# Kernel optimization log

Measured on AMD Instinct MI355X. Metric: run time of the kernel, lower is better.

## Reference

```python
import jax, jax.numpy as jnp
import numpy as np

HEADS, MAX_SEQ, N_STATE = 8, 2048, 512
DEPTH = N_STATE // HEADS
B, S = 2, 2048
EPS = 1e-5


def setup_inputs() -> dict:
    key = jax.random.key(0)
    ks = jax.random.split(key, 8)
    sd = lambda f: 1.0 / np.sqrt(f)
    causal = jnp.tril(jnp.ones((S, S), dtype=bool))
    mask = jnp.where(causal, 0.0, -1e9).astype(jnp.float32)[None, None]
    return {
        "x": jax.random.normal(ks[0], (B, S, N_STATE), jnp.float32),
        "mask": mask,
        "W_qkv": jax.random.normal(ks[1], (N_STATE, 3 * N_STATE), jnp.float32) * sd(N_STATE),
        "b_qkv": jnp.zeros((3 * N_STATE,), jnp.float32),
        "W_proj": jax.random.normal(ks[2], (N_STATE, N_STATE), jnp.float32) * sd(N_STATE),
        "b_proj": jnp.zeros((N_STATE,), jnp.float32),
        "E": jax.random.normal(ks[3], (HEADS, MAX_SEQ, DEPTH), jnp.float32) * sd(DEPTH),
        "g1": jnp.ones((N_STATE,), jnp.float32),
        "be1": jnp.zeros((N_STATE,), jnp.float32),
        "g2": jnp.ones((N_STATE,), jnp.float32),
        "be2": jnp.zeros((N_STATE,), jnp.float32),
        "W_fc1": jax.random.normal(ks[4], (N_STATE, 4 * N_STATE), jnp.float32) * sd(N_STATE),
        "b_fc1": jnp.zeros((4 * N_STATE,), jnp.float32),
        "W_fc2": jax.random.normal(ks[5], (4 * N_STATE, N_STATE), jnp.float32) * sd(4 * N_STATE),
        "b_fc2": jnp.zeros((N_STATE,), jnp.float32),
    }


def _layernorm(x, g, b):
    mu = jnp.mean(x, axis=-1, keepdims=True)
    var = jnp.mean(jnp.square(x - mu), axis=-1, keepdims=True)
    return (x - mu) * jax.lax.rsqrt(var + EPS) * g + b


def _relative_skew(rel):
    # rel: [B, H, S, S] = q @ E_slice^T ; skew trick -> relative positions
    b, h, s, _ = rel.shape
    rel = jnp.pad(rel, ((0, 0), (0, 0), (0, 0), (1, 0)))  # [B,H,S,S+1]
    rel = rel.reshape(b, h, s + 1, s)
    return rel[:, :, 1:, :]  # [B,H,S,S]


def reference(x, mask, W_qkv, b_qkv, W_proj, b_proj, E, g1, be1, g2, be2,
              W_fc1, b_fc1, W_fc2, b_fc2):
    b, s, _ = x.shape
    a = _layernorm(x, g1, be1)
    qkv = a @ W_qkv + b_qkv  # [B,S,3N]
    q, k, v = jnp.split(qkv, 3, axis=-1)
    split = lambda t: t.reshape(b, s, HEADS, DEPTH).transpose(0, 2, 1, 3)  # [B,H,S,D]
    q, k, v = split(q), split(k), split(v)
    present = jnp.stack([k, v], axis=1)  # [B,2,H,S,D]

    w = jnp.einsum("bhqd,bhkd->bhqk", q, k)
    E_s = E[:, MAX_SEq if False else MAX_SEQ - s:, :]  # [H,S,D]
    rel = jnp.einsum("bhqd,hld->bhql", q, E_s)
    w = (w + _relative_skew(rel)) * (1.0 / np.sqrt(DEPTH))
    w = w + mask
    w = jax.nn.softmax(w, axis=-1)
    att = jnp.einsum("bhqk,bhkd->bhqd", w, v)
    att = att.transpose(0, 2, 1, 3).reshape(b, s, N_STATE)
    att = att @ W_proj + b_proj

    x = x + att
    m = _layernorm(x, g2, be2)
    m = jax.nn.gelu(m @ W_fc1 + b_fc1) @ W_fc2 + b_fc2
    x = x + m
    return (x, present)
```

## Files before the change

kernel.cpp:

```cpp
#include <hip/hip_runtime.h>
#include <stdint.h>

#define DEV __device__ __forceinline__

typedef __attribute__((ext_vector_type(8))) short bf16x8;
typedef __attribute__((ext_vector_type(4))) float f32x4;

DEV ushort f2bf(float f) {
  union { float f; uint32_t u; } c; c.f = f;
  return (ushort)((c.u + 0x7FFFu + ((c.u >> 16) & 1)) >> 16);
}
DEV bf16x8 ld8(const ushort* p) { return *reinterpret_cast<const bf16x8*>(p); }

DEV void gload16(const void* g, void* l) {
  __builtin_amdgcn_global_load_lds(
      (const __attribute__((address_space(1))) uint32_t*)g,
      (__attribute__((address_space(3))) uint32_t*)l, 16, 0, 0);
}

__global__ __launch_bounds__(256) void k_transpose_bf(const float* __restrict__ in,
                                                      ushort* __restrict__ out,
                                                      int R, int C) {
  __shared__ float t[32][33];
  int tx = threadIdx.x & 31, ty = threadIdx.x >> 5;
  int c0 = blockIdx.x * 32, r0 = blockIdx.y * 32;
#pragma unroll
  for (int k = 0; k < 4; ++k)
    t[ty + 8 * k][tx] = in[(size_t)(r0 + ty + 8 * k) * C + c0 + tx];
  __syncthreads();
#pragma unroll
  for (int k = 0; k < 4; ++k)
    out[(size_t)(c0 + ty + 8 * k) * R + r0 + tx] = f2bf(t[tx][ty + 8 * k]);
}

__global__ __launch_bounds__(256) void k_cvt_bf(const float* __restrict__ in,
                                                ushort* __restrict__ out, int n4) {
  int i = blockIdx.x * 256 + threadIdx.x;
  if (i >= n4) return;
  float4 v = reinterpret_cast<const float4*>(in)[i];
  ushort4 o; o.x = f2bf(v.x); o.y = f2bf(v.y); o.z = f2bf(v.z); o.w = f2bf(v.w);
  reinterpret_cast<ushort4*>(out)[i] = o;
}

__global__ __launch_bounds__(256) void k_ln(const float* __restrict__ x,
                                            const float* __restrict__ g,
                                            const float* __restrict__ be,
                                            ushort* __restrict__ out) {
  int w = threadIdx.x >> 6, lane = threadIdx.x & 63;
  int row = blockIdx.x * 4 + w;
  const float* xr = x + (size_t)row * 512 + lane * 8;
  float4 a = *reinterpret_cast<const float4*>(xr);
  float4 b = *reinterpret_cast<const float4*>(xr + 4);
  float xs[8] = {a.x, a.y, a.z, a.w, b.x, b.y, b.z, b.w};
  float s = 0.f, q = 0.f;
#pragma unroll
  for (int i = 0; i < 8; ++i) { s += xs[i]; q += xs[i] * xs[i]; }
#pragma unroll
  for (int off = 32; off; off >>= 1) { s += __shfl_xor(s, off); q += __shfl_xor(q, off); }
  float mu = s * (1.f / 512.f);
  float var = q * (1.f / 512.f) - mu * mu;
  float inv = rsqrtf(var + 1e-5f);
  const float* gp = g + lane * 8;
  const float* bp = be + lane * 8;
  ushort o[8];
#pragma unroll
  for (int i = 0; i < 8; ++i) o[i] = f2bf((xs[i] - mu) * inv * gp[i] + bp[i]);
  *reinterpret_cast<uint4*>(out + (size_t)row * 512 + lane * 8) = *reinterpret_cast<uint4*>(o);
}

template <int EPI, int BN>
__global__ __launch_bounds__(256) void k_gemm(
    const ushort* __restrict__ A, const ushort* __restrict__ Bt,
    int M, int N, int K,
    const float* __restrict__ bias, const float* __restrict__ res,
    float* __restrict__ outf, ushort* __restrict__ outb,
    float* __restrict__ present, ushort* __restrict__ qbf,
    ushort* __restrict__ kbf, ushort* __restrict__ vtbf) {
  constexpr int NF = BN / 32;
  __shared__ ushort As[2][128][64];
  __shared__ ushort Bs[2][BN][64];
  const int tid = threadIdx.x, lane = tid & 63, w = tid >> 6;
  const int g = lane >> 4, l16 = lane & 15;
  const int m0 = blockIdx.y * 128, n0 = blockIdx.x * BN;
  const int wm = (w >> 1) * 64, wn = (w & 1) * (BN / 2);
  f32x4 acc[4][NF];
#pragma unroll
  for (int i = 0; i < 4; ++i)
#pragma unroll
    for (int j = 0; j < NF; ++j) acc[i][j] = (f32x4){0.f, 0.f, 0.f, 0.f};

  const int lrow_off = (lane << 4);
  auto stage = [&](int buf, int k0) {
#pragma unroll
    for (int sw = 0; sw < 4; ++sw) {
      int offb = sw * 4096 + w * 1024;
      int loff = offb + lrow_off;
      int row = loff >> 7, colb = loff & 127;
      gload16((const char*)A + (((size_t)(m0 + row) * K + k0) << 1) + colb,
              (char*)(&As[buf][0][0]) + offb);
    }
#pragma unroll
    for (int sw = 0; sw < BN / 32; ++sw) {
      int offb = sw * 4096 + w * 1024;
      int loff = offb + lrow_off;
      int row = loff >> 7, colb = loff & 127;
      gload16((const char*)Bt + (((size_t)(n0 + row) * K + k0) << 1) + colb,
              (char*)(&Bs[buf][0][0]) + offb);
    }
  };

  const int nt = K >> 6;
  stage(0, 0);
  __syncthreads();
  for (int t = 0; t < nt; ++t) {
    const int cur = t & 1;
    if (t + 1 < nt) stage(cur ^ 1, (t + 1) << 6);
#pragma unroll
    for (int kk = 0; kk < 2; ++kk) {
      bf16x8 af[4], bfr[NF];
#pragma unroll
      for (int f = 0; f < 4; ++f)
        af[f] = *reinterpret_cast<const bf16x8*>(&As[cur][wm + f * 16 + l16][kk * 32 + g * 8]);
#pragma unroll
      for (int f = 0; f < NF; ++f)
        bfr[f] = *reinterpret_cast<const bf16x8*>(&Bs[cur][wn + f * 16 + l16][kk * 32 + g * 8]);
#pragma unroll
      for (int i = 0; i < 4; ++i)
#pragma unroll
        for (int j = 0; j < NF; ++j)
          acc[i][j] = __builtin_amdgcn_mfma_f32_16x16x32_bf16(af[i], bfr[j], acc[i][j], 0, 0, 0);
    }
    __syncthreads();
  }

#pragma unroll
  for (int i = 0; i < 4; ++i)
#pragma unroll
    for (int j = 0; j < NF; ++j)
#pragma unroll
      for (int r = 0; r < 4; ++r) {
        int row = m0 + wm + i * 16 + g * 4 + r;
        int col = n0 + wn + j * 16 + l16;
        float v = acc[i][j][r] + bias[col];
        if constexpr (EPI == 0) {
          int third = col >> 9, hh = (col >> 6) & 7, d = col & 63;
          int bb = row >> 11, sq = row & 2047;
          if (third == 0) {
            qbf[((((size_t)bb * 8 + hh) * 2048) + sq) * 64 + d] = f2bf(v);
          } else {
            present[((((size_t)bb * 2 + (third - 1)) * 8 + hh) * 2048 + sq) * 64 + d] = v;
            if (third == 1)
              kbf[((((size_t)bb * 8 + hh) * 2048) + sq) * 64 + d] = f2bf(v);
            else
              vtbf[(((size_t)bb * 8 + hh) * 64 + d) * 2048 + sq] = f2bf(v);
          }
        } else if constexpr (EPI == 1) {
          size_t idx = (size_t)row * N + col;
          outf[idx] = v + res[idx];
        } else {
          float u = 0.7978845608f * (v + 0.044715f * v * v * v);
          float e = __expf(2.f * u);
          float th = 1.f - 2.f / (e + 1.f);
          outb[(size_t)row * N + col] = f2bf(0.5f * v * (1.f + th));
        }
      }
}

__global__ __launch_bounds__(128, 2) void k_attn(
    const ushort* __restrict__ qbf, const ushort* __restrict__ kbf,
    const ushort* __restrict__ vtbf, const ushort* __restrict__ Ebf,
    ushort* __restrict__ attb) {
  constexpr int S = 2048;
  __shared__ ushort Ps[2][16][76];
  __shared__ float Mrg[64][24];
  const int tid = threadIdx.x, lane = tid & 63, ks = tid >> 6;
  const int g = lane >> 4, l16 = lane & 15;
  const int bid = blockIdx.x;
  const int h = bid & 7, rest = bid >> 3;
  const int b = rest & 1, t = 127 - (rest >> 1);
  const int bh = b * 8 + h;

  const ushort* qp = qbf + (size_t)bh * S * 64;
  const ushort* kp = kbf + (size_t)bh * S * 64;
  const ushort* vp = vtbf + (size_t)bh * 64 * S;
  const ushort* ep = Ebf + (size_t)h * S * 64;

  const int i0 = t * 16;
  bf16x8 qf[2];
  qf[0] = ld8(qp + (size_t)(i0 + l16) * 64 + g * 8);
  qf[1] = ld8(qp + (size_t)(i0 + l16) * 64 + 32 + g * 8);
  f32x4 o[4];
#pragma unroll
  for (int fv = 0; fv < 4; ++fv) o[fv] = (f32x4){0.f, 0.f, 0.f, 0.f};
  float mrun[4], lrun[4];
#pragma unroll
  for (int r = 0; r < 4; ++r) { mrun[r] = -1e30f; lrun[r] = 0.f; }
  const int nkt = (t + 4) >> 2;

  for (int kt = ks; kt < nkt; kt += 2) {
    const int j0 = kt * 64;
    const int tb = S - 16 - i0 + j0;
    bf16x8 kf[8], ef[10], vf[8];
#pragma unroll
    for (int fn = 0; fn < 4; ++fn) {
      const ushort* kr = kp + (size_t)(j0 + fn * 16 + l16) * 64 + g * 8;
      kf[fn] = ld8(kr);
      kf[4 + fn] = ld8(kr + 32);
    }
#pragma unroll
    for (int fc = 0; fc < 5; ++fc) {
      int l = tb + fc * 16 + l16; if (l > S - 1) l = S - 1;
      const ushort* er = ep + (size_t)l * 64 + g * 8;
      ef[fc] = ld8(er);
      ef[5 + fc] = ld8(er + 32);
    }
#pragma unroll
    for (int fv = 0; fv < 4; ++fv) {
      const ushort* vr = vp + (size_t)(fv * 16 + l16) * S + j0 + g * 8;
      vf[fv] = ld8(vr);
      vf[4 + fv] = ld8(vr + 32);
    }

    f32x4 sacc[4];
#pragma unroll
    for (int fn = 0; fn < 4; ++fn) sacc[fn] = (f32x4){0.f, 0.f, 0.f, 0.f};
#pragma unroll
    for (int kk = 0; kk < 2; ++kk)
#pragma unroll
      for (int fn = 0; fn < 4; ++fn)
        sacc[fn] = __builtin_amdgcn_mfma_f32_16x16x32_bf16(qf[kk], kf[kk * 4 + fn], sacc[fn], 0, 0, 0);

    f32x4 racc[5];
#pragma unroll
    for (int fc = 0; fc < 5; ++fc) racc[fc] = (f32x4){0.f, 0.f, 0.f, 0.f};
#pragma unroll
    for (int kk = 0; kk < 2; ++kk)
#pragma unroll
      for (int fc = 0; fc < 5; ++fc)
        racc[fc] = __builtin_amdgcn_mfma_f32_16x16x32_bf16(qf[kk], ef[kk * 5 + fc], racc[fc], 0, 0, 0);

    float Sv[4][4], mtile[4];
#pragma unroll
    for (int r = 0; r < 4; ++r) mtile[r] = -1e30f;
#pragma unroll
    for (int r = 0; r < 4; ++r) {
      const int dr = g * 4 + r;
      const int src = (lane & 48) | ((l16 + 15 - dr) & 15);
      const bool hi = (l16 > dr);
#pragma unroll
      for (int fn = 0; fn < 4; ++fn) {
        float lo_v = __shfl(racc[fn][r], src);
        float hi_v = __shfl(racc[fn + 1][r], src);
        float rel = hi ? hi_v : lo_v;
        float sv = (sacc[fn][r] + rel) * 0.125f;
        int dj = fn * 16 + l16;
        if (j0 + dj > i0 + dr) sv = -1e30f;
        Sv[fn][r] = sv;
        mtile[r] = fmaxf(mtile[r], sv);
      }
    }
#pragma unroll
    for (int off = 1; off < 16; off <<= 1)
#pragma unroll
      for (int r = 0; r < 4; ++r) mtile[r] = fmaxf(mtile[r], __shfl_xor(mtile[r], off));
    float corr[4], psum[4];
#pragma unroll
    for (int r = 0; r < 4; ++r) {
      float mn = fmaxf(mrun[r], mtile[r]);
      corr[r] = __expf(mrun[r] - mn);
      mrun[r] = mn;
      psum[r] = 0.f;
    }
#pragma unroll
    for (int fn = 0; fn < 4; ++fn)
#pragma unroll
      for (int r = 0; r < 4; ++r) {
        float pv = __expf(Sv[fn][r] - mrun[r]);
        psum[r] += pv;
        Ps[ks][g * 4 + r][fn * 16 + l16] = f2bf(pv);
      }
#pragma unroll
    for (int off = 1; off < 16; off <<= 1)
#pragma unroll
      for (int r = 0; r < 4; ++r) psum[r] += __shfl_xor(psum[r], off);
#pragma unroll
    for (int r = 0; r < 4; ++r) lrun[r] = lrun[r] * corr[r] + psum[r];
#pragma unroll
    for (int fv = 0; fv < 4; ++fv)
#pragma unroll
      for (int r = 0; r < 4; ++r) o[fv][r] *= corr[r];

#pragma unroll
    for (int kk = 0; kk < 2; ++kk) {
      bf16x8 pf = ld8(&Ps[ks][l16][kk * 32 + g * 8]);
#pragma unroll
      for (int fv = 0; fv < 4; ++fv)
        o[fv] = __builtin_amdgcn_mfma_f32_16x16x32_bf16(pf, vf[kk * 4 + fv], o[fv], 0, 0, 0);
    }
  }

  if (ks == 1) {
    float* mb = &Mrg[lane][0];
#pragma unroll
    for (int fv = 0; fv < 4; ++fv)
#pragma unroll
      for (int r = 0; r < 4; ++r) mb[fv * 4 + r] = o[fv][r];
#pragma unroll
    for (int r = 0; r < 4; ++r) { mb[16 + r] = mrun[r]; mb[20 + r] = lrun[r]; }
  }
  __syncthreads();
  if (ks == 0) {
    const float* mb = &Mrg[lane][0];
#pragma unroll
    for (int r = 0; r < 4; ++r) {
      float m1 = mb[16 + r];
      float mm = fmaxf(mrun[r], m1);
      float e0 = __expf(mrun[r] - mm), e1 = __expf(m1 - mm);
      float lc = lrun[r] * e0 + mb[20 + r] * e1;
      float inv = 1.f / lc;
#pragma unroll
      for (int fv = 0; fv < 4; ++fv) {
        float oc = o[fv][r] * e0 + mb[fv * 4 + r] * e1;
        attb[(size_t)(b * S + i0 + g * 4 + r) * 512 + h * 64 + fv * 16 + l16] =
            f2bf(oc * inv);
      }
    }
  }
}

extern "C" void kernel_launch(void* const* d_in, const int* in_sizes, int n_in,
                              void* d_out, int out_size, void* d_ws, size_t ws_size,
                              hipStream_t stream) {
  const float* x = (const float*)d_in[0];
  const float* W_qkv = (const float*)d_in[2];
  const float* b_qkv = (const float*)d_in[3];
  const float* W_proj = (const float*)d_in[4];
  const float* b_proj = (const float*)d_in[5];
  const float* E = (const float*)d_in[6];
  const float* g1 = (const float*)d_in[7];
  const float* be1 = (const float*)d_in[8];
  const float* g2 = (const float*)d_in[9];
  const float* be2 = (const float*)d_in[10];
  const float* W_fc1 = (const float*)d_in[11];
  const float* b_fc1 = (const float*)d_in[12];
  const float* W_fc2 = (const float*)d_in[13];
  const float* b_fc2 = (const float*)d_in[14];

  float* x_out = (float*)d_out;
  float* present = x_out + 2097152;

  char* ws = (char*)d_ws;
  ushort* a_bf   = (ushort*)(ws + 0);
  ushort* m_bf   = (ushort*)(ws + 4194304);
  ushort* q_bf   = (ushort*)(ws + 8388608);
  ushort* att_bf = (ushort*)(ws + 12582912);
  ushort* h_bf   = (ushort*)(ws + 16777216);
  ushort* k_bf   = (ushort*)(ws + 16777216);
  ushort* vt_bf  = (ushort*)(ws + 20971520);
  float*  x2     = (float*)(ws + 33554432);
  ushort* Wqkv_t = (ushort*)(ws + 41943040);
  ushort* Wproj_t= (ushort*)(ws + 43515904);
  ushort* Wfc1_t = (ushort*)(ws + 44040192);
  ushort* Wfc2_t = (ushort*)(ws + 46137344);
  ushort* E_bf   = (ushort*)(ws + 48234496);

  k_transpose_bf<<<dim3(48, 16), 256, 0, stream>>>(W_qkv, Wqkv_t, 512, 1536);
  k_transpose_bf<<<dim3(16, 16), 256, 0, stream>>>(W_proj, Wproj_t, 512, 512);
  k_transpose_bf<<<dim3(64, 16), 256, 0, stream>>>(W_fc1, Wfc1_t, 512, 2048);
  k_transpose_bf<<<dim3(16, 64), 256, 0, stream>>>(W_fc2, Wfc2_t, 2048, 512);
  k_cvt_bf<<<1024, 256, 0, stream>>>(E, E_bf, 262144);
  k_ln<<<1024, 256, 0, stream>>>(x, g1, be1, a_bf);
  k_gemm<0, 128><<<dim3(12, 32), 256, 0, stream>>>(a_bf, Wqkv_t, 4096, 1536, 512,
                                                   b_qkv, nullptr, nullptr, nullptr,
                                                   present, q_bf, k_bf, vt_bf);
  k_attn<<<2048, 128, 0, stream>>>(q_bf, k_bf, vt_bf, E_bf, att_bf);
  k_gemm<1, 64><<<dim3(8, 32), 256, 0, stream>>>(att_bf, Wproj_t, 4096, 512, 512,
                                                 b_proj, x, x2, nullptr, nullptr, nullptr,
                                                 nullptr, nullptr);
  k_ln<<<1024, 256, 0, stream>>>(x2, g2, be2, m_bf);
  k_gemm<2, 128><<<dim3(16, 32), 256, 0, stream>>>(m_bf, Wfc1_t, 4096, 2048, 512,
                                                   b_fc1, nullptr, nullptr, h_bf, nullptr,
                                                   nullptr, nullptr, nullptr);
  k_gemm<1, 64><<<dim3(8, 32), 256, 0, stream>>>(h_bf, Wfc2_t, 4096, 512, 2048,
                                                 b_fc2, x2, x_out, nullptr, nullptr, nullptr,
                                                 nullptr, nullptr);
}
```

Baseline: 322.4 us.

## Prefetch GEMM tiles two stages ahead with explicit vmcnt waits and barriers

Restructures the bf16 GEMM main loop so global-to-LDS loads are issued two K-tiles ahead instead of one. Each iteration reads all LDS fragments into registers, barriers, refills the freed buffer with tile t+2, then runs the MFMAs and waits only on the older loads through partial s_waitcnt vmcnt counts. This aims to hide global load latency behind compute and to drop a full __syncthreads drain per tile. The cost is more registers for fragments, hand-tuned wait counts that must match the per-thread load count, and scheduling barriers that constrain the compiler; a sched barrier is also added in the attention kernel.

```diff
diff --git a/kernel.cpp b/kernel.cpp
--- a/kernel.cpp
+++ b/kernel.cpp
@@ -2,6 +2,9 @@
 #include <stdint.h>
 
 #define DEV __device__ __forceinline__
+#define SCHEDB __builtin_amdgcn_sched_barrier(0)
+#define WAITVM(n) asm volatile("s_waitcnt vmcnt(" #n ")" ::: "memory")
+#define WAITLG asm volatile("s_waitcnt lgkmcnt(0)" ::: "memory")
 
 typedef __attribute__((ext_vector_type(8))) short bf16x8;
 typedef __attribute__((ext_vector_type(4))) float f32x4;
@@ -77,6 +80,7 @@
     float* __restrict__ present, ushort* __restrict__ qbf,
     ushort* __restrict__ kbf, ushort* __restrict__ vtbf) {
   constexpr int NF = BN / 32;
+  constexpr int LOADS = 4 + BN / 32;
   __shared__ ushort As[2][128][64];
   __shared__ ushort Bs[2][BN][64];
   const int tid = threadIdx.x, lane = tid & 63, w = tid >> 6;
@@ -111,26 +115,51 @@
 
   const int nt = K >> 6;
   stage(0, 0);
-  __syncthreads();
+  stage(1, 64);
+  if constexpr (LOADS == 8) WAITVM(8); else WAITVM(6);
+  SCHEDB;
+  __builtin_amdgcn_s_barrier();
+  SCHEDB;
+
   for (int t = 0; t < nt; ++t) {
     const int cur = t & 1;
-    if (t + 1 < nt) stage(cur ^ 1, (t + 1) << 6);
+    bf16x8 af[2][4], bfr[2][NF];
 #pragma unroll
     for (int kk = 0; kk < 2; ++kk) {
-      bf16x8 af[4], bfr[NF];
 #pragma unroll
       for (int f = 0; f < 4; ++f)
-        af[f] = *reinterpret_cast<const bf16x8*>(&As[cur][wm + f * 16 + l16][kk * 32 + g * 8]);
+        af[kk][f] = *reinterpret_cast<const bf16x8*>(
+            &As[cur][wm + f * 16 + l16][kk * 32 + g * 8]);
 #pragma unroll
       for (int f = 0; f < NF; ++f)
-        bfr[f] = *reinterpret_cast<const bf16x8*>(&Bs[cur][wn + f * 16 + l16][kk * 32 + g * 8]);
+        bfr[kk][f] = *reinterpret_cast<const bf16x8*>(
+            &Bs[cur][wn + f * 16 + l16][kk * 32 + g * 8]);
+    }
+    WAITLG;
+    SCHEDB;
+    __builtin_amdgcn_s_barrier();
+    SCHEDB;
+    if (t + 2 < nt) stage(cur, (t + 2) << 6);
+    SCHEDB;
+#pragma unroll
+    for (int kk = 0; kk < 2; ++kk)
 #pragma unroll
       for (int i = 0; i < 4; ++i)
 #pragma unroll
         for (int j = 0; j < NF; ++j)
-          acc[i][j] = __builtin_amdgcn_mfma_f32_16x16x32_bf16(af[i], bfr[j], acc[i][j], 0, 0, 0);
-    }
-    __syncthreads();
+          acc[i][j] = __builtin_amdgcn_mfma_f32_16x16x32_bf16(
+              af[kk][i], bfr[kk][j], acc[i][j], 0, 0, 0);
+    SCHEDB;
+    if (t + 1 < nt) {
+      if (t + 2 < nt) {
+        if constexpr (LOADS == 8) WAITVM(8); else WAITVM(6);
+      } else {
+        WAITVM(0);
+      }
+      SCHEDB;
+      __builtin_amdgcn_s_barrier();
+      SCHEDB;
+    }
   }
 
 #pragma unroll
@@ -220,6 +249,7 @@
       vf[fv] = ld8(vr);
       vf[4 + fv] = ld8(vr + 32);
     }
+    SCHEDB;
 
     f32x4 sacc[4];
 #pragma unroll
```

New measurement: 312.1 us. 3.2% less time.
